# Performance work log

Measured on AMD Instinct MI355X. Metric: run time of the kernel, lower is better.

The kernel has to match this reference:

```python
import jax, jax.numpy as jnp
import numpy as np

# Whisper-small decoder, prefill path (text_offset == 0, no KV caches)
L, D, H, V, NCTX, S_AUDIO, B, T, MAXC = 12, 768, 12, 51865, 448, 1500, 2, 192, 256
DH = D // H
SCALE = DH ** -0.5
EPS = 1e-5

PNAMES = ['attn_ln_g', 'attn_ln_b', 'attn_q_w', 'attn_q_b', 'attn_k_w', 'attn_v_w', 'attn_v_b',
          'attn_o_w', 'attn_o_b', 'cross_ln_g', 'cross_ln_b', 'cross_q_w', 'cross_q_b',
          'cross_k_w', 'cross_v_w', 'cross_v_b', 'cross_o_w', 'cross_o_b',
          'mlp_ln_g', 'mlp_ln_b', 'mlp_w1', 'mlp_b1', 'mlp_w2', 'mlp_b2', 'ln_g', 'ln_b']


def _ln(x, g, b):
    m = jnp.mean(x, -1, keepdims=True)
    v = jnp.mean((x - m) ** 2, -1, keepdims=True)
    return (x - m) * jax.lax.rsqrt(v + EPS) * g + b


def _heads(t):
    b, t_, _ = t.shape
    return t.reshape(b, t_, H, DH).transpose(0, 2, 1, 3)  # (b,H,t,DH)


def _mha(q, k, v, mask):
    qh, kh, vh = _heads(q), _heads(k), _heads(v)
    qk = jnp.matmul(qh, kh.swapaxes(-1, -2)) * SCALE  # (B,H,Tq,Tk), broadcasts over kv batch 1
    if mask is not None:
        qk = qk + mask
    w = jax.nn.softmax(qk, axis=-1)
    o = jnp.matmul(w, vh)  # (B,H,Tq,DH)
    o = o.transpose(0, 2, 1, 3).reshape(q.shape[0], q.shape[1], D)
    return o, qk


def _lin(x, w, b=None):
    y = jnp.einsum('bti,oi->bto', x, w)
    return y if b is None else y + b


def _forward(x, xa, tok_emb, pos_emb, P):
    h = tok_emb[x] + pos_emb[:T]                        # (B,T,D)
    h = jnp.pad(h, ((0, 0), (0, MAXC - T), (0, 0)))     # pad to max_n_ctx_for_1st=256
    r = jnp.arange(MAXC)
    mask = jnp.where((r[None, :] > r[:, None]) | (r[None, :] >= T), -jnp.inf, 0.0)
    xa1 = xa[:1]                                        # xa.split(1)[0] in torch
    cross_qks, new_mkv, new_ckv = [], [], []
    for l in range(L):
        y = _ln(h, P['attn_ln_g'][l], P['attn_ln_b'][l])
        q = _lin(y, P['attn_q_w'][l], P['attn_q_b'][l])
        k = _lin(y, P['attn_k_w'][l])
        v = _lin(y, P['attn_v_w'][l], P['attn_v_b'][l])
        new_mkv += [k, v]
        o, _ = _mha(q, k, v, mask)
        h = h + _lin(o, P['attn_o_w'][l], P['attn_o_b'][l])
        y = _ln(h, P['cross_ln_g'][l], P['cross_ln_b'][l])
        q = _lin(y, P['cross_q_w'][l], P['cross_q_b'][l])
        ck = _lin(xa1, P['cross_k_w'][l])
        cv = _lin(xa1, P['cross_v_w'][l], P['cross_v_b'][l])
        new_ckv += [ck, cv]
        o, cqk = _mha(q, ck, cv, None)
        cross_qks.append(jax.lax.stop_gradient(cqk))    # qk.detach() in torch
        h = h + _lin(o, P['cross_o_w'][l], P['cross_o_b'][l])
        y = _ln(h, P['mlp_ln_g'][l], P['mlp_ln_b'][l])
        h = h + _lin(jax.nn.gelu(_lin(y, P['mlp_w1'][l], P['mlp_b1'][l]), approximate=False),
                     P['mlp_w2'][l], P['mlp_b2'][l])
    h = _ln(h, P['ln_g'], P['ln_b'])
    logits = jnp.matmul(h[:, :T], tok_emb.T).astype(jnp.float32)       # (B,T,V)
    cross_qks = jnp.concatenate(cross_qks, axis=0)[:, :, :T, :]        # (L*B,H,T,S_AUDIO)
    return logits, cross_qks, jnp.stack(new_mkv), jnp.stack(new_ckv)


def setup_inputs() -> dict:
    key = jax.random.key(0)
    ks = iter(jax.random.split(key, 48))
    def p(shape, s=0.02):
        return jax.random.normal(next(ks), shape, jnp.float32) * s
    inp = {
        'x': jax.random.randint(next(ks), (B, T), 0, V, dtype=jnp.int32),
        'xa': jax.random.normal(next(ks), (B, S_AUDIO, D), jnp.float32),
        'text_offset': 0,
        'isNewCKV': 1,
        'tok_emb': p((V, D)),
        'pos_emb': p((NCTX, D)),
        'attn_ln_g': 1.0 + p((L, D)), 'attn_ln_b': p((L, D)),
        'attn_q_w': p((L, D, D)), 'attn_q_b': p((L, D)),
        'attn_k_w': p((L, D, D)),
        'attn_v_w': p((L, D, D)), 'attn_v_b': p((L, D)),
        'attn_o_w': p((L, D, D)), 'attn_o_b': p((L, D)),
        'cross_ln_g': 1.0 + p((L, D)), 'cross_ln_b': p((L, D)),
        'cross_q_w': p((L, D, D)), 'cross_q_b': p((L, D)),
        'cross_k_w': p((L, D, D)),
        'cross_v_w': p((L, D, D)), 'cross_v_b': p((L, D)),
        'cross_o_w': p((L, D, D)), 'cross_o_b': p((L, D)),
        'mlp_ln_g': 1.0 + p((L, D)), 'mlp_ln_b': p((L, D)),
        'mlp_w1': p((L, 4 * D, D)), 'mlp_b1': p((L, 4 * D)),
        'mlp_w2': p((L, D, 4 * D)), 'mlp_b2': p((L, D)),
        'ln_g': 1.0 + p((D,)), 'ln_b': p((D,)),
    }
    return inp


def reference(x, xa, text_offset, isNewCKV, tok_emb, pos_emb,
              attn_ln_g, attn_ln_b, attn_q_w, attn_q_b, attn_k_w, attn_v_w, attn_v_b,
              attn_o_w, attn_o_b, cross_ln_g, cross_ln_b, cross_q_w, cross_q_b,
              cross_k_w, cross_v_w, cross_v_b, cross_o_w, cross_o_b,
              mlp_ln_g, mlp_ln_b, mlp_w1, mlp_b1, mlp_w2, mlp_b2, ln_g, ln_b):
    # text_offset == 0 prefill path; isNewCKV unused in the pure-python torch path
    P = dict(zip(PNAMES, (attn_ln_g, attn_ln_b, attn_q_w, attn_q_b, attn_k_w, attn_v_w, attn_v_b,
                          attn_o_w, attn_o_b, cross_ln_g, cross_ln_b, cross_q_w, cross_q_b,
                          cross_k_w, cross_v_w, cross_v_b, cross_o_w, cross_o_b,
                          mlp_ln_g, mlp_ln_b, mlp_w1, mlp_b1, mlp_w2, mlp_b2, ln_g, ln_b)))
    return _forward(x, xa, tok_emb, pos_emb, P)
```

## Files before the change

kernel.cpp:

```cpp
#include <hip/hip_runtime.h>
#include <math.h>

constexpr int kL = 12, kD = 768, kH = 12, kV = 51865, kSA = 1500;
constexpr int kB = 2, kT = 192, kMC = 256, kDH = 64;
constexpr float kScale = 0.125f;
constexpr float kEps = 1e-5f;
constexpr int kR = kB * kMC;
constexpr int kSLDc = 1504;

constexpr size_t SZ_LOGITS = (size_t)kB * kT * kV;
constexpr size_t SZ_CQK    = (size_t)kL * kB * kH * kT * kSA;
constexpr size_t SZ_MKV    = (size_t)2 * kL * kB * kMC * kD;
constexpr size_t OFF_CQK = SZ_LOGITS;
constexpr size_t OFF_MKV = OFF_CQK + SZ_CQK;
constexpr size_t OFF_CKV = OFF_MKV + SZ_MKV;

typedef float f32x4v __attribute__((ext_vector_type(4)));
typedef unsigned short us8v __attribute__((ext_vector_type(8)));
typedef unsigned short us4v __attribute__((ext_vector_type(4)));
typedef unsigned int   u32x4 __attribute__((ext_vector_type(4)));

static __device__ __forceinline__ unsigned short f2bf(float f) {
    unsigned int u = __float_as_uint(f);
    u += 0x7fffu + ((u >> 16) & 1u);
    return (unsigned short)(u >> 16);
}

static __device__ __forceinline__ unsigned int f2bf2(float lo, float hi) {
    unsigned int r;
    asm("v_cvt_pk_bf16_f32 %0, %1, %2" : "=v"(r) : "v"(lo), "v"(hi));
    return r;
}

static __device__ __forceinline__ float bf2f(unsigned short u) {
    return __uint_as_float((unsigned int)u << 16);
}

static __device__ __forceinline__ f32x4v mfma_bf16(us8v a, us8v b, f32x4v c) {
    asm("v_mfma_f32_16x16x32_bf16 %0, %1, %2, %0" : "+v"(c) : "v"(a), "v"(b));
    return c;
}

__global__ void k_embed(const int* __restrict__ x, const float* __restrict__ tok,
                        const float* __restrict__ pos, float* __restrict__ h)
{
    int idx = blockIdx.x * 256 + threadIdx.x;
    int d = idx % kD;
    int t = (idx / kD) % kMC;
    int b = idx / (kD * kMC);
    float v = 0.f;
    if (t < kT) {
        int tokid = x[b * kT + t];
        v = tok[(size_t)tokid * kD + d] + pos[(size_t)t * kD + d];
    }
    h[idx] = v;
}

__global__ void k_ln(const float* __restrict__ in, const float* __restrict__ g,
                     const float* __restrict__ bb, unsigned short* __restrict__ out)
{
    int r = blockIdx.x;
    const float* xr = in + (size_t)r * kD;
    int t = threadIdx.x;
    float x0 = xr[t], x1 = xr[t + 256], x2 = xr[t + 512];
    float s  = x0 + x1 + x2;
    float sq = x0 * x0 + x1 * x1 + x2 * x2;
    __shared__ float red[8];
    for (int o = 32; o > 0; o >>= 1) { s += __shfl_down(s, o); sq += __shfl_down(sq, o); }
    int w = t >> 6;
    if ((t & 63) == 0) { red[w] = s; red[4 + w] = sq; }
    __syncthreads();
    s  = red[0] + red[1] + red[2] + red[3];
    sq = red[4] + red[5] + red[6] + red[7];
    float m   = s * (1.f / kD);
    float var = sq * (1.f / kD) - m * m;
    float rs  = rsqrtf(var + kEps);
    unsigned short* orow = out + (size_t)r * kD;
    orow[t]       = f2bf((x0 - m) * rs * g[t]       + bb[t]);
    orow[t + 256] = f2bf((x1 - m) * rs * g[t + 256] + bb[t + 256]);
    orow[t + 512] = f2bf((x2 - m) * rs * g[t + 512] + bb[t + 512]);
}

__global__ void k_finalln(const float* __restrict__ h, const float* __restrict__ g,
                          const float* __restrict__ bb, unsigned short* __restrict__ out)
{
    int r = blockIdx.x;
    int b = r / kT, tt = r % kT;
    const float* xr = h + (size_t)(b * kMC + tt) * kD;
    int t = threadIdx.x;
    float x0 = xr[t], x1 = xr[t + 256], x2 = xr[t + 512];
    float s  = x0 + x1 + x2;
    float sq = x0 * x0 + x1 * x1 + x2 * x2;
    __shared__ float red[8];
    for (int o = 32; o > 0; o >>= 1) { s += __shfl_down(s, o); sq += __shfl_down(sq, o); }
    int w = t >> 6;
    if ((t & 63) == 0) { red[w] = s; red[4 + w] = sq; }
    __syncthreads();
    s  = red[0] + red[1] + red[2] + red[3];
    sq = red[4] + red[5] + red[6] + red[7];
    float m   = s * (1.f / kD);
    float var = sq * (1.f / kD) - m * m;
    float rs  = rsqrtf(var + kEps);
    unsigned short* orow = out + (size_t)r * kD;
    orow[t]       = f2bf((x0 - m) * rs * g[t]       + bb[t]);
    orow[t + 256] = f2bf((x1 - m) * rs * g[t + 256] + bb[t + 256]);
    orow[t + 512] = f2bf((x2 - m) * rs * g[t + 512] + bb[t + 512]);
}

struct GEntry { const float* W; const float* bias; const float* res; void* out; };
struct GBatch { GEntry e[24]; };

template <int ABF, int OBF>
__global__ __launch_bounds__(256)
void gemm_t(const void* __restrict__ Av, GBatch gb, int M, int N, int K,
            int dogelu)
{
    constexpr int LD = 72;
    __shared__ unsigned short As[3][64][LD];
    __shared__ unsigned short Ws[3][64][LD];
    const GEntry ge = gb.e[blockIdx.z];
    const float* __restrict__ W = ge.W;
    int bn = blockIdx.y * 64;
    int bm = blockIdx.x * 64;
    int tid = threadIdx.x;
    int wid = tid >> 6, lane = tid & 63;
    int wm = (wid >> 1) * 32, wn = (wid & 1) * 32;
    int l15 = lane & 15, lg = lane >> 4;
    int r = tid >> 2, cq = (tid & 3) * 16;
    int gr = bm + r, gc = bn + r;

    auto load_a = [&](int k0, u32x4& p0, u32x4& p1) {
        p0 = (u32x4){}; p1 = (u32x4){};
        if (ABF) {
            if (gr < M) {
                const unsigned short* ar =
                    (const unsigned short*)Av + (size_t)gr * K + k0 + cq;
                p0 = *(const u32x4*)ar;
                p1 = *(const u32x4*)(ar + 8);
            }
        } else {
            if (gr < M) {
                const float* ar = (const float*)Av + (size_t)gr * K + k0 + cq;
                float4 v0 = *(const float4*)(ar);
                float4 v1 = *(const float4*)(ar + 4);
                float4 v2 = *(const float4*)(ar + 8);
                float4 v3 = *(const float4*)(ar + 12);
                p0[0] = f2bf2(v0.x, v0.y); p0[1] = f2bf2(v0.z, v0.w);
                p0[2] = f2bf2(v1.x, v1.y); p0[3] = f2bf2(v1.z, v1.w);
                p1[0] = f2bf2(v2.x, v2.y); p1[1] = f2bf2(v2.z, v2.w);
                p1[2] = f2bf2(v3.x, v3.y); p1[3] = f2bf2(v3.z, v3.w);
            }
        }
    };
    auto load_w = [&](int k0, u32x4& p0, u32x4& p1) {
        p0 = (u32x4){}; p1 = (u32x4){};
        if (gc < N) {
            const float* wr = W + (size_t)gc * K + k0 + cq;
            float4 v0 = *(const float4*)(wr);
            float4 v1 = *(const float4*)(wr + 4);
            float4 v2 = *(const float4*)(wr + 8);
            float4 v3 = *(const float4*)(wr + 12);
            p0[0] = f2bf2(v0.x, v0.y); p0[1] = f2bf2(v0.z, v0.w);
            p0[2] = f2bf2(v1.x, v1.y); p0[3] = f2bf2(v1.z, v1.w);
            p1[0] = f2bf2(v2.x, v2.y); p1[1] = f2bf2(v2.z, v2.w);
            p1[2] = f2bf2(v3.x, v3.y); p1[3] = f2bf2(v3.z, v3.w);
        }
    };
    auto stage = [&](int buf, u32x4 a0, u32x4 a1, u32x4 w0, u32x4 w1) {
        *(u32x4*)&As[buf][r][cq]     = a0;
        *(u32x4*)&As[buf][r][cq + 8] = a1;
        *(u32x4*)&Ws[buf][r][cq]     = w0;
        *(u32x4*)&Ws[buf][r][cq + 8] = w1;
    };

    f32x4v acc00 = {}, acc01 = {}, acc10 = {}, acc11 = {};
    auto domfma = [&](int buf) {
        #pragma unroll
        for (int kc = 0; kc < 2; ++kc) {
            us8v af0 = *(const us8v*)&As[buf][wm + l15][kc * 32 + lg * 8];
            us8v af1 = *(const us8v*)&As[buf][wm + 16 + l15][kc * 32 + lg * 8];
            us8v wf0 = *(const us8v*)&Ws[buf][wn + l15][kc * 32 + lg * 8];
            us8v wf1 = *(const us8v*)&Ws[buf][wn + 16 + l15][kc * 32 + lg * 8];
            acc00 = mfma_bf16(af0, wf0, acc00);
            acc01 = mfma_bf16(af0, wf1, acc01);
            acc10 = mfma_bf16(af1, wf0, acc10);
            acc11 = mfma_bf16(af1, wf1, acc11);
        }
    };

    u32x4 a0A, a1A, w0A, w1A, a0B, a1B, w0B, w1B;
    load_a(0, a0A, a1A); load_w(0, w0A, w1A);
    stage(0, a0A, a1A, w0A, w1A);
    load_a(64, a0B, a1B); load_w(64, w0B, w1B);
    __syncthreads();

    int cur = 0;
    for (int k0 = 0; k0 < K; k0 += 128) {
        int n1 = cur + 1; if (n1 == 3) n1 = 0;
        int n2 = n1 + 1; if (n2 == 3) n2 = 0;
        if (k0 + 128 < K) { load_a(k0 + 128, a0A, a1A); load_w(k0 + 128, w0A, w1A); }
        domfma(cur);
        stage(n1, a0B, a1B, w0B, w1B);
        __syncthreads();
        if (k0 + 192 < K) { load_a(k0 + 192, a0B, a1B); load_w(k0 + 192, w0B, w1B); }
        domfma(n1);
        if (k0 + 128 < K) {
            stage(n2, a0A, a1A, w0A, w1A);
            __syncthreads();
        }
        cur = n2;
    }

    const float* bias = ge.bias;
    const float* res  = ge.res;
    f32x4v accs[2][2] = { { acc00, acc01 }, { acc10, acc11 } };
    #pragma unroll
    for (int fi = 0; fi < 2; ++fi) {
        #pragma unroll
        for (int fj = 0; fj < 2; ++fj) {
            int col = bn + wn + fj * 16 + l15;
            if (col >= N) continue;
            float bv = bias ? bias[col] : 0.f;
            #pragma unroll
            for (int rr = 0; rr < 4; ++rr) {
                int row = bm + wm + fi * 16 + lg * 4 + rr;
                if (row >= M) continue;
                float v = accs[fi][fj][rr] + bv;
                if (dogelu) v = 0.5f * v * (1.f + erff(v * 0.70710678118654752f));
                if (OBF) {
                    ((unsigned short*)ge.out)[(size_t)row * N + col] = f2bf(v);
                } else {
                    if (res) v += res[(size_t)row * N + col];
                    ((float*)ge.out)[(size_t)row * N + col] = v;
                }
            }
        }
    }
}

__global__ __launch_bounds__(256)
void k_logits(const unsigned short* __restrict__ A, const float* __restrict__ W,
              float* __restrict__ out)
{
    constexpr int LD = 72;
    __shared__ unsigned short As[64][LD];
    __shared__ unsigned short Ws[2][64][LD];
    int bn = blockIdx.x * 64;
    int tid = threadIdx.x;
    int wid = tid >> 6, lane = tid & 63;
    int wm = (wid >> 1) * 32, wn = (wid & 1) * 32;
    int l15 = lane & 15, lg = lane >> 4;
    int r = tid >> 2, cq = (tid & 3) * 16;
    int gc = bn + r;

    auto load_w = [&](int k0, u32x4& p0, u32x4& p1) {
        p0 = (u32x4){}; p1 = (u32x4){};
        if (gc < kV) {
            const float* wr = W + (size_t)gc * kD + k0 + cq;
            float4 v0 = *(const float4*)(wr);
            float4 v1 = *(const float4*)(wr + 4);
            float4 v2 = *(const float4*)(wr + 8);
            float4 v3 = *(const float4*)(wr + 12);
            p0[0] = f2bf2(v0.x, v0.y); p0[1] = f2bf2(v0.z, v0.w);
            p0[2] = f2bf2(v1.x, v1.y); p0[3] = f2bf2(v1.z, v1.w);
            p1[0] = f2bf2(v2.x, v2.y); p1[1] = f2bf2(v2.z, v2.w);
            p1[2] = f2bf2(v3.x, v3.y); p1[3] = f2bf2(v3.z, v3.w);
        }
    };

    f32x4v acc[6][4];
    #pragma unroll
    for (int i = 0; i < 6; ++i)
        #pragma unroll
        for (int j = 0; j < 4; ++j) acc[i][j] = (f32x4v){};

    u32x4 rw0, rw1;
    load_w(0, rw0, rw1);
    *(u32x4*)&Ws[0][r][cq]     = rw0;
    *(u32x4*)&Ws[0][r][cq + 8] = rw1;
    __syncthreads();

    int cur = 0;
    for (int k0 = 0; k0 < kD; k0 += 64) {
        bool more = (k0 + 64) < kD;
        if (more) load_w(k0 + 64, rw0, rw1);
        #pragma unroll
        for (int mt = 0; mt < 6; ++mt) {
            {
                const unsigned short* ar = A + (size_t)(mt * 64 + r) * kD + k0 + cq;
                us8v v0 = *(const us8v*)ar;
                us8v v1 = *(const us8v*)(ar + 8);
                *(us8v*)&As[r][cq]     = v0;
                *(us8v*)&As[r][cq + 8] = v1;
            }
            __syncthreads();
            #pragma unroll
            for (int kc = 0; kc < 2; ++kc) {
                us8v af0 = *(const us8v*)&As[wm + l15][kc * 32 + lg * 8];
                us8v af1 = *(const us8v*)&As[wm + 16 + l15][kc * 32 + lg * 8];
                us8v wf0 = *(const us8v*)&Ws[cur][wn + l15][kc * 32 + lg * 8];
                us8v wf1 = *(const us8v*)&Ws[cur][wn + 16 + l15][kc * 32 + lg * 8];
                acc[mt][0] = mfma_bf16(af0, wf0, acc[mt][0]);
                acc[mt][1] = mfma_bf16(af0, wf1, acc[mt][1]);
                acc[mt][2] = mfma_bf16(af1, wf0, acc[mt][2]);
                acc[mt][3] = mfma_bf16(af1, wf1, acc[mt][3]);
            }
            __syncthreads();
        }
        if (more) {
            int nxt = cur ^ 1;
            *(u32x4*)&Ws[nxt][r][cq]     = rw0;
            *(u32x4*)&Ws[nxt][r][cq + 8] = rw1;
            cur = nxt;
        }
    }
    #pragma unroll
    for (int mt = 0; mt < 6; ++mt) {
        #pragma unroll
        for (int fi = 0; fi < 2; ++fi) {
            #pragma unroll
            for (int fj = 0; fj < 2; ++fj) {
                int col = bn + wn + fj * 16 + l15;
                if (col >= kV) continue;
                #pragma unroll
                for (int rr = 0; rr < 4; ++rr) {
                    int row = mt * 64 + wm + fi * 16 + lg * 4 + rr;
                    out[(size_t)row * kV + col] = acc[mt][fi * 2 + fj][rr];
                }
            }
        }
    }
}

template <int QBF>
__global__ __launch_bounds__(256)
void k_scores(const void* __restrict__ qv, const float* __restrict__ kk,
              unsigned short* __restrict__ sws, float* __restrict__ cqk,
              int Nk, int sld, int selfmask, int kPerB)
{
    constexpr int LD = 72;
    __shared__ unsigned short As[64][LD];
    __shared__ unsigned short Ks[64][LD];
    int z = blockIdx.z, b = z / kH, h = z % kH;
    int bm = blockIdx.x * 64, bn = blockIdx.y * 64;
    const float* kbase = kk + (kPerB ? (size_t)b * kMC * kD : 0) + (size_t)h * kDH;

    int tid = threadIdx.x;
    int r = tid >> 2, c0 = (tid & 3) * 16;
    {
        if (QBF) {
            const unsigned short* q = (const unsigned short*)qv;
            const unsigned short* qr =
                q + (size_t)(b * kMC + bm + r) * kD + h * kDH + c0;
            *(us8v*)&As[r][c0]     = *(const us8v*)qr;
            *(us8v*)&As[r][c0 + 8] = *(const us8v*)(qr + 8);
        } else {
            const float* q = (const float*)qv;
            const float* qr = q + (size_t)(b * kMC + bm + r) * kD + h * kDH + c0;
            float4 v0 = *(const float4*)(qr);
            float4 v1 = *(const float4*)(qr + 4);
            float4 v2 = *(const float4*)(qr + 8);
            float4 v3 = *(const float4*)(qr + 12);
            u32x4 p0, p1;
            p0[0] = f2bf2(v0.x, v0.y); p0[1] = f2bf2(v0.z, v0.w);
            p0[2] = f2bf2(v1.x, v1.y); p0[3] = f2bf2(v1.z, v1.w);
            p1[0] = f2bf2(v2.x, v2.y); p1[1] = f2bf2(v2.z, v2.w);
            p1[2] = f2bf2(v3.x, v3.y); p1[3] = f2bf2(v3.z, v3.w);
            *(u32x4*)&As[r][c0]     = p0;
            *(u32x4*)&As[r][c0 + 8] = p1;
        }
        int gk = bn + r;
        if (gk < Nk) {
            const float* kr = kbase + (size_t)gk * kD + c0;
            float4 v0 = *(const float4*)(kr);
            float4 v1 = *(const float4*)(kr + 4);
            float4 v2 = *(const float4*)(kr + 8);
            float4 v3 = *(const float4*)(kr + 12);
            u32x4 p0, p1;
            p0[0] = f2bf2(v0.x, v0.y); p0[1] = f2bf2(v0.z, v0.w);
            p0[2] = f2bf2(v1.x, v1.y); p0[3] = f2bf2(v1.z, v1.w);
            p1[0] = f2bf2(v2.x, v2.y); p1[1] = f2bf2(v2.z, v2.w);
            p1[2] = f2bf2(v3.x, v3.y); p1[3] = f2bf2(v3.z, v3.w);
            *(u32x4*)&Ks[r][c0]     = p0;
            *(u32x4*)&Ks[r][c0 + 8] = p1;
        } else {
            u32x4 zz = {};
            *(u32x4*)&Ks[r][c0]     = zz;
            *(u32x4*)&Ks[r][c0 + 8] = zz;
        }
    }
    __syncthreads();

    int wid = tid >> 6, lane = tid & 63;
    int wm = (wid >> 1) * 32, wn = (wid & 1) * 32;
    int l15 = lane & 15, lg = lane >> 4;

    f32x4v acc[2][2] = {};
    #pragma unroll
    for (int kc = 0; kc < 2; ++kc) {
        us8v a0 = *(const us8v*)&As[wm + l15][kc * 32 + lg * 8];
        us8v a1 = *(const us8v*)&As[wm + 16 + l15][kc * 32 + lg * 8];
        us8v b0 = *(const us8v*)&Ks[wn + l15][kc * 32 + lg * 8];
        us8v b1 = *(const us8v*)&Ks[wn + 16 + l15][kc * 32 + lg * 8];
        acc[0][0] = mfma_bf16(a0, b0, acc[0][0]);
        acc[0][1] = mfma_bf16(a0, b1, acc[0][1]);
        acc[1][0] = mfma_bf16(a1, b0, acc[1][0]);
        acc[1][1] = mfma_bf16(a1, b1, acc[1][1]);
    }

    #pragma unroll
    for (int fm = 0; fm < 2; ++fm) {
        #pragma unroll
        for (int fn = 0; fn < 2; ++fn) {
            int gj = bn + wn + fn * 16 + l15;
            if (gj >= Nk) continue;
            #pragma unroll
            for (int rr = 0; rr < 4; ++rr) {
                int gi = bm + wm + fm * 16 + lg * 4 + rr;
                float val = acc[fm][fn][rr] * kScale;
                if (cqk && gi < kT)
                    cqk[(((size_t)(b * kH + h)) * kT + gi) * kSA + gj] = val;
                if (selfmask && (gj > gi || gj >= kT)) val = -1e30f;
                sws[((size_t)z * kMC + gi) * sld + gj] = f2bf(val);
            }
        }
    }
}

constexpr int kCH  = 128;
constexpr int kLDK = 136;
__global__ __launch_bounds__(256)
void k_pv(const unsigned short* __restrict__ sws, const float* __restrict__ vv,
          unsigned short* __restrict__ o, int Nk, int sld, int vPerB)
{
    __shared__ unsigned short Pb[16][kLDK];
    __shared__ unsigned short Vt[64][kLDK];
    __shared__ float smx[16], sinv[16];
    int z = blockIdx.y, b = z / kH, h = z % kH;
    int i0 = blockIdx.x * 16;
    int t = threadIdx.x, wid = t >> 6, lane = t & 63;
    int l15 = lane & 15, lg = lane >> 4;
    const float* vbase = vv + (vPerB ? (size_t)b * kMC * kD : 0) + (size_t)h * kDH;

    for (int r2 = wid; r2 < 16; r2 += 4) {
        const unsigned short* srow2 = sws + ((size_t)z * kMC + i0 + r2) * sld;
        float mx = -3e38f;
        for (int j0 = lane * 8; j0 < Nk; j0 += 512) {
            us8v v = *(const us8v*)&srow2[j0];
            #pragma unroll
            for (int e = 0; e < 8; ++e)
                if (j0 + e < Nk) mx = fmaxf(mx, bf2f(v[e]));
        }
        for (int off = 32; off > 0; off >>= 1) mx = fmaxf(mx, __shfl_xor(mx, off));
        float sum = 0.f;
        for (int j0 = lane * 8; j0 < Nk; j0 += 512) {
            us8v v = *(const us8v*)&srow2[j0];
            #pragma unroll
            for (int e = 0; e < 8; ++e)
                if (j0 + e < Nk) sum += expf(bf2f(v[e]) - mx);
        }
        for (int off = 32; off > 0; off >>= 1) sum += __shfl_xor(sum, off);
        if (lane == 0) { smx[r2] = mx; sinv[r2] = 1.f / sum; }
    }
    __syncthreads();

    int pr = t >> 4;
    int jb = (t & 15) * 8;
    const unsigned short* srow = sws + ((size_t)z * kMC + i0 + pr) * sld;
    float mxv = smx[pr];

    f32x4v acc = {};
    for (int k0 = 0; k0 < Nk; k0 += kCH) {
        #pragma unroll
        for (int u = 0; u < 4; ++u) {
            int flat = t + u * 256;
            int kr = (flat >> 4) * 2;
            int c4 = flat & 15;
            float4 va = {0,0,0,0}, vb2 = {0,0,0,0};
            if (k0 + kr < Nk)
                va = *(const float4*)(vbase + (size_t)(k0 + kr) * kD + c4 * 4);
            if (k0 + kr + 1 < Nk)
                vb2 = *(const float4*)(vbase + (size_t)(k0 + kr + 1) * kD + c4 * 4);
            *(unsigned int*)&Vt[c4 * 4 + 0][kr] = f2bf2(va.x, vb2.x);
            *(unsigned int*)&Vt[c4 * 4 + 1][kr] = f2bf2(va.y, vb2.y);
            *(unsigned int*)&Vt[c4 * 4 + 2][kr] = f2bf2(va.z, vb2.z);
            *(unsigned int*)&Vt[c4 * 4 + 3][kr] = f2bf2(va.w, vb2.w);
        }
        {
            us8v praw = *(const us8v*)&srow[k0 + jb];
            #pragma unroll
            for (int u = 0; u < 8; u += 2) {
                int gj0 = k0 + jb + u;
                float e0 = (gj0     < Nk) ? expf(bf2f(praw[u])     - mxv) : 0.f;
                float e1 = (gj0 + 1 < Nk) ? expf(bf2f(praw[u + 1]) - mxv) : 0.f;
                *(unsigned int*)&Pb[pr][jb + u] = f2bf2(e0, e1);
            }
        }
        __syncthreads();
        #pragma unroll
        for (int kc = 0; kc < 4; ++kc) {
            us8v a  = *(const us8v*)&Pb[l15][kc * 32 + lg * 8];
            us8v bf = *(const us8v*)&Vt[wid * 16 + l15][kc * 32 + lg * 8];
            acc = mfma_bf16(a, bf, acc);
        }
        __syncthreads();
    }

    #pragma unroll
    for (int rr = 0; rr < 4; ++rr) {
        int row = lg * 4 + rr;
        float v = acc[rr] * sinv[row];
        o[(size_t)(b * kMC + i0 + row) * kD + h * kDH + wid * 16 + l15] = f2bf(v);
    }
}

extern "C" void kernel_launch(void* const* d_in, const int* in_sizes, int n_in,
                              void* d_out, int out_size, void* d_ws, size_t ws_size,
                              hipStream_t stream)
{
    const int*   x   = (const int*)  d_in[0];
    const float* xa  = (const float*)d_in[1];
    const float* tok = (const float*)d_in[4];
    const float* pos = (const float*)d_in[5];
    const float* attn_ln_g  = (const float*)d_in[6];
    const float* attn_ln_b  = (const float*)d_in[7];
    const float* attn_q_w   = (const float*)d_in[8];
    const float* attn_q_b   = (const float*)d_in[9];
    const float* attn_k_w   = (const float*)d_in[10];
    const float* attn_v_w   = (const float*)d_in[11];
    const float* attn_v_b   = (const float*)d_in[12];
    const float* attn_o_w   = (const float*)d_in[13];
    const float* attn_o_b   = (const float*)d_in[14];
    const float* cross_ln_g = (const float*)d_in[15];
    const float* cross_ln_b = (const float*)d_in[16];
    const float* cross_q_w  = (const float*)d_in[17];
    const float* cross_q_b  = (const float*)d_in[18];
    const float* cross_k_w  = (const float*)d_in[19];
    const float* cross_v_w  = (const float*)d_in[20];
    const float* cross_v_b  = (const float*)d_in[21];
    const float* cross_o_w  = (const float*)d_in[22];
    const float* cross_o_b  = (const float*)d_in[23];
    const float* mlp_ln_g   = (const float*)d_in[24];
    const float* mlp_ln_b   = (const float*)d_in[25];
    const float* mlp_w1     = (const float*)d_in[26];
    const float* mlp_b1     = (const float*)d_in[27];
    const float* mlp_w2     = (const float*)d_in[28];
    const float* mlp_b2     = (const float*)d_in[29];
    const float* ln_g       = (const float*)d_in[30];
    const float* ln_b       = (const float*)d_in[31];

    float* out = (float*)d_out;
    float* h    = (float*)d_ws;
    float* qws  = h   + (size_t)kR * kD;
    unsigned short* sS    = (unsigned short*)(qws + (size_t)kR * kD);
    unsigned short* y16   = sS   + (size_t)kB * kH * kMC * kSLDc;
    unsigned short* qb16  = y16  + (size_t)kR * kD;
    unsigned short* o16   = qb16 + (size_t)kR * kD;
    unsigned short* hid16 = o16  + (size_t)kR * kD;
    unsigned short* yF16  = hid16 + (size_t)kR * 4 * kD;

    k_embed<<<kB * kMC * kD / 256, 256, 0, stream>>>(x, tok, pos, h);

    {
        GBatch gc{};
        for (int l = 0; l < kL; ++l) {
            gc.e[2 * l]     = { cross_k_w + (size_t)l * kD * kD, nullptr, nullptr,
                                out + OFF_CKV + (size_t)(2 * l) * kSA * kD };
            gc.e[2 * l + 1] = { cross_v_w + (size_t)l * kD * kD, cross_v_b + (size_t)l * kD,
                                nullptr,
                                out + OFF_CKV + (size_t)(2 * l + 1) * kSA * kD };
        }
        gemm_t<0, 0><<<dim3((kSA + 63) / 64, kD / 64, 2 * kL), 256, 0, stream>>>(
            xa, gc, kSA, kD, kD, 0);
    }

    for (int l = 0; l < kL; ++l) {
        size_t dd = (size_t)l * kD * kD;
        float* kbuf  = out + OFF_MKV + (size_t)(2 * l)     * kB * kMC * kD;
        float* vbuf  = out + OFF_MKV + (size_t)(2 * l + 1) * kB * kMC * kD;
        float* ckbuf = out + OFF_CKV + (size_t)(2 * l)     * kSA * kD;
        float* cvbuf = out + OFF_CKV + (size_t)(2 * l + 1) * kSA * kD;
        float* cqk   = out + OFF_CQK + (size_t)l * kB * kH * kT * kSA;

        k_ln<<<kR, 256, 0, stream>>>(h, attn_ln_g + l * kD, attn_ln_b + l * kD, y16);
        {
            GBatch g3{};
            g3.e[0] = { attn_q_w + dd, attn_q_b + (size_t)l * kD, nullptr, qws };
            g3.e[1] = { attn_k_w + dd, nullptr,                   nullptr, kbuf };
            g3.e[2] = { attn_v_w + dd, attn_v_b + (size_t)l * kD, nullptr, vbuf };
            gemm_t<1, 0><<<dim3(kR / 64, kD / 64, 3), 256, 0, stream>>>(
                y16, g3, kR, kD, kD, 0);
        }
        k_scores<0><<<dim3(kMC / 64, kMC / 64, kB * kH), 256, 0, stream>>>(
            qws, kbuf, sS, nullptr, kMC, kMC, 1, 1);
        k_pv<<<dim3(kMC / 16, kB * kH), 256, 0, stream>>>(sS, vbuf, o16, kMC, kMC, 1);
        {
            GBatch g1{};
            g1.e[0] = { attn_o_w + dd, attn_o_b + (size_t)l * kD, h, h };
            gemm_t<1, 0><<<dim3(kR / 64, kD / 64, 1), 256, 0, stream>>>(
                o16, g1, kR, kD, kD, 0);
        }

        k_ln<<<kR, 256, 0, stream>>>(h, cross_ln_g + l * kD, cross_ln_b + l * kD, y16);
        {
            GBatch g1{};
            g1.e[0] = { cross_q_w + dd, cross_q_b + (size_t)l * kD, nullptr, qb16 };
            gemm_t<1, 1><<<dim3(kR / 64, kD / 64, 1), 256, 0, stream>>>(
                y16, g1, kR, kD, kD, 0);
        }
        k_scores<1><<<dim3(kMC / 64, (kSA + 63) / 64, kB * kH), 256, 0, stream>>>(
            qb16, ckbuf, sS, cqk, kSA, kSLDc, 0, 0);
        k_pv<<<dim3(kMC / 16, kB * kH), 256, 0, stream>>>(sS, cvbuf, o16, kSA, kSLDc, 0);
        {
            GBatch g1{};
            g1.e[0] = { cross_o_w + dd, cross_o_b + (size_t)l * kD, h, h };
            gemm_t<1, 0><<<dim3(kR / 64, kD / 64, 1), 256, 0, stream>>>(
                o16, g1, kR, kD, kD, 0);
        }

        k_ln<<<kR, 256, 0, stream>>>(h, mlp_ln_g + l * kD, mlp_ln_b + l * kD, y16);
        {
            GBatch g1{};
            g1.e[0] = { mlp_w1 + (size_t)l * 4 * kD * kD, mlp_b1 + (size_t)l * 4 * kD,
                        nullptr, hid16 };
            gemm_t<1, 1><<<dim3(kR / 64, 4 * kD / 64, 1), 256, 0, stream>>>(
                y16, g1, kR, 4 * kD, kD, 1);
        }
        {
            GBatch g1{};
            g1.e[0] = { mlp_w2 + (size_t)l * 4 * kD * kD, mlp_b2 + (size_t)l * kD, h, h };
            gemm_t<1, 0><<<dim3(kR / 64, kD / 64, 1), 256, 0, stream>>>(
                hid16, g1, kR, kD, 4 * kD, 0);
        }
    }

    k_finalln<<<kB * kT, 256, 0, stream>>>(h, ln_g, ln_b, yF16);
    k_logits<<<dim3((kV + 63) / 64), 256, 0, stream>>>(yF16, tok, out);
}
```

Measured before the change: 3.325 ms.

## Split cross-attn scores kernel with K-tile reuse across query tiles; widen PV row blocks

Adds a dedicated cross-attention scores kernel where each block loads and converts one 64-row K tile once and loops over all four query tiles, instead of reloading and reconverting K per query tile. The self-attention scores kernel is specialised with the masking and strides fixed. The PV kernel now processes 32 query rows per block with two MFMA accumulators that share each V tile, halving the V reload and conversion work. The risks are lower parallelism (fewer blocks) and serialized query-tile loops with extra syncs.

```diff
diff --git a/kernel.cpp b/kernel.cpp
--- a/kernel.cpp
+++ b/kernel.cpp
@@ -332,62 +332,45 @@
     }
 }
 
-template <int QBF>
 __global__ __launch_bounds__(256)
-void k_scores(const void* __restrict__ qv, const float* __restrict__ kk,
-              unsigned short* __restrict__ sws, float* __restrict__ cqk,
-              int Nk, int sld, int selfmask, int kPerB)
+void k_scores(const float* __restrict__ q, const float* __restrict__ kk,
+              unsigned short* __restrict__ sws)
 {
     constexpr int LD = 72;
     __shared__ unsigned short As[64][LD];
     __shared__ unsigned short Ks[64][LD];
     int z = blockIdx.z, b = z / kH, h = z % kH;
     int bm = blockIdx.x * 64, bn = blockIdx.y * 64;
-    const float* kbase = kk + (kPerB ? (size_t)b * kMC * kD : 0) + (size_t)h * kDH;
+    const float* kbase = kk + (size_t)b * kMC * kD + (size_t)h * kDH;
 
     int tid = threadIdx.x;
     int r = tid >> 2, c0 = (tid & 3) * 16;
     {
-        if (QBF) {
-            const unsigned short* q = (const unsigned short*)qv;
-            const unsigned short* qr =
-                q + (size_t)(b * kMC + bm + r) * kD + h * kDH + c0;
-            *(us8v*)&As[r][c0]     = *(const us8v*)qr;
-            *(us8v*)&As[r][c0 + 8] = *(const us8v*)(qr + 8);
-        } else {
-            const float* q = (const float*)qv;
-            const float* qr = q + (size_t)(b * kMC + bm + r) * kD + h * kDH + c0;
-            float4 v0 = *(const float4*)(qr);
-            float4 v1 = *(const float4*)(qr + 4);
-            float4 v2 = *(const float4*)(qr + 8);
-            float4 v3 = *(const float4*)(qr + 12);
-            u32x4 p0, p1;
-            p0[0] = f2bf2(v0.x, v0.y); p0[1] = f2bf2(v0.z, v0.w);
-            p0[2] = f2bf2(v1.x, v1.y); p0[3] = f2bf2(v1.z, v1.w);
-            p1[0] = f2bf2(v2.x, v2.y); p1[1] = f2bf2(v2.z, v2.w);
-            p1[2] = f2bf2(v3.x, v3.y); p1[3] = f2bf2(v3.z, v3.w);
-            *(u32x4*)&As[r][c0]     = p0;
-            *(u32x4*)&As[r][c0 + 8] = p1;
-        }
-        int gk = bn + r;
-        if (gk < Nk) {
-            const float* kr = kbase + (size_t)gk * kD + c0;
-            float4 v0 = *(const float4*)(kr);
-            float4 v1 = *(const float4*)(kr + 4);
-            float4 v2 = *(const float4*)(kr + 8);
-            float4 v3 = *(const float4*)(kr + 12);
-            u32x4 p0, p1;
-            p0[0] = f2bf2(v0.x, v0.y); p0[1] = f2bf2(v0.z, v0.w);
-            p0[2] = f2bf2(v1.x, v1.y); p0[3] = f2bf2(v1.z, v1.w);
-            p1[0] = f2bf2(v2.x, v2.y); p1[1] = f2bf2(v2.z, v2.w);
-            p1[2] = f2bf2(v3.x, v3.y); p1[3] = f2bf2(v3.z, v3.w);
-            *(u32x4*)&Ks[r][c0]     = p0;
-            *(u32x4*)&Ks[r][c0 + 8] = p1;
-        } else {
-            u32x4 zz = {};
-            *(u32x4*)&Ks[r][c0]     = zz;
-            *(u32x4*)&Ks[r][c0 + 8] = zz;
-        }
+        const float* qr = q + (size_t)(b * kMC + bm + r) * kD + h * kDH + c0;
+        float4 v0 = *(const float4*)(qr);
+        float4 v1 = *(const float4*)(qr + 4);
+        float4 v2 = *(const float4*)(qr + 8);
+        float4 v3 = *(const float4*)(qr + 12);
+        u32x4 p0, p1;
+        p0[0] = f2bf2(v0.x, v0.y); p0[1] = f2bf2(v0.z, v0.w);
+        p0[2] = f2bf2(v1.x, v1.y); p0[3] = f2bf2(v1.z, v1.w);
+        p1[0] = f2bf2(v2.x, v2.y); p1[1] = f2bf2(v2.z, v2.w);
+        p1[2] = f2bf2(v3.x, v3.y); p1[3] = f2bf2(v3.z, v3.w);
+        *(u32x4*)&As[r][c0]     = p0;
+        *(u32x4*)&As[r][c0 + 8] = p1;
+
+        const float* kr = kbase + (size_t)(bn + r) * kD + c0;
+        float4 k0 = *(const float4*)(kr);
+        float4 k1 = *(const float4*)(kr + 4);
+        float4 k2 = *(const float4*)(kr + 8);
+        float4 k3 = *(const float4*)(kr + 12);
+        u32x4 q0, q1;
+        q0[0] = f2bf2(k0.x, k0.y); q0[1] = f2bf2(k0.z, k0.w);
+        q0[2] = f2bf2(k1.x, k1.y); q0[3] = f2bf2(k1.z, k1.w);
+        q1[0] = f2bf2(k2.x, k2.y); q1[1] = f2bf2(k2.z, k2.w);
+        q1[2] = f2bf2(k3.x, k3.y); q1[3] = f2bf2(k3.z, k3.w);
+        *(u32x4*)&Ks[r][c0]     = q0;
+        *(u32x4*)&Ks[r][c0 + 8] = q1;
     }
     __syncthreads();
 
@@ -413,17 +396,94 @@
         #pragma unroll
         for (int fn = 0; fn < 2; ++fn) {
             int gj = bn + wn + fn * 16 + l15;
-            if (gj >= Nk) continue;
             #pragma unroll
             for (int rr = 0; rr < 4; ++rr) {
                 int gi = bm + wm + fm * 16 + lg * 4 + rr;
                 float val = acc[fm][fn][rr] * kScale;
-                if (cqk && gi < kT)
-                    cqk[(((size_t)(b * kH + h)) * kT + gi) * kSA + gj] = val;
-                if (selfmask && (gj > gi || gj >= kT)) val = -1e30f;
-                sws[((size_t)z * kMC + gi) * sld + gj] = f2bf(val);
-            }
-        }
+                if (gj > gi || gj >= kT) val = -1e30f;
+                sws[((size_t)z * kMC + gi) * kMC + gj] = f2bf(val);
+            }
+        }
+    }
+}
+
+__global__ __launch_bounds__(256)
+void k_xscores(const unsigned short* __restrict__ q, const float* __restrict__ ck,
+               unsigned short* __restrict__ sws, float* __restrict__ cqk)
+{
+    constexpr int LD = 72;
+    __shared__ unsigned short As[64][LD];
+    __shared__ unsigned short Ks[64][LD];
+    int z = blockIdx.y, b = z / kH, h = z % kH;
+    int bn = blockIdx.x * 64;
+    int tid = threadIdx.x;
+    int wid = tid >> 6, lane = tid & 63;
+    int wm = (wid >> 1) * 32, wn = (wid & 1) * 32;
+    int l15 = lane & 15, lg = lane >> 4;
+    int r = tid >> 2, c0 = (tid & 3) * 16;
+
+    {
+        int gk = bn + r;
+        if (gk < kSA) {
+            const float* kr = ck + (size_t)gk * kD + h * kDH + c0;
+            float4 k0 = *(const float4*)(kr);
+            float4 k1 = *(const float4*)(kr + 4);
+            float4 k2 = *(const float4*)(kr + 8);
+            float4 k3 = *(const float4*)(kr + 12);
+            u32x4 q0, q1;
+            q0[0] = f2bf2(k0.x, k0.y); q0[1] = f2bf2(k0.z, k0.w);
+            q0[2] = f2bf2(k1.x, k1.y); q0[3] = f2bf2(k1.z, k1.w);
+            q1[0] = f2bf2(k2.x, k2.y); q1[1] = f2bf2(k2.z, k2.w);
+            q1[2] = f2bf2(k3.x, k3.y); q1[3] = f2bf2(k3.z, k3.w);
+            *(u32x4*)&Ks[r][c0]     = q0;
+            *(u32x4*)&Ks[r][c0 + 8] = q1;
+        } else {
+            u32x4 zz = {};
+            *(u32x4*)&Ks[r][c0]     = zz;
+            *(u32x4*)&Ks[r][c0 + 8] = zz;
+        }
+    }
+
+    for (int mt = 0; mt < 4; ++mt) {
+        int bm = mt * 64;
+        {
+            const unsigned short* qr =
+                q + (size_t)(b * kMC + bm + r) * kD + h * kDH + c0;
+            *(us8v*)&As[r][c0]     = *(const us8v*)qr;
+            *(us8v*)&As[r][c0 + 8] = *(const us8v*)(qr + 8);
+        }
+        __syncthreads();
+
+        f32x4v acc[2][2] = {};
+        #pragma unroll
+        for (int kc = 0; kc < 2; ++kc) {
+            us8v a0 = *(const us8v*)&As[wm + l15][kc * 32 + lg * 8];
+            us8v a1 = *(const us8v*)&As[wm + 16 + l15][kc * 32 + lg * 8];
+            us8v b0 = *(const us8v*)&Ks[wn + l15][kc * 32 + lg * 8];
+            us8v b1 = *(const us8v*)&Ks[wn + 16 + l15][kc * 32 + lg * 8];
+            acc[0][0] = mfma_bf16(a0, b0, acc[0][0]);
+            acc[0][1] = mfma_bf16(a0, b1, acc[0][1]);
+            acc[1][0] = mfma_bf16(a1, b0, acc[1][0]);
+            acc[1][1] = mfma_bf16(a1, b1, acc[1][1]);
+        }
+
+        #pragma unroll
+        for (int fm = 0; fm < 2; ++fm) {
+            #pragma unroll
+            for (int fn = 0; fn < 2; ++fn) {
+                int gj = bn + wn + fn * 16 + l15;
+                if (gj >= kSA) continue;
+                #pragma unroll
+                for (int rr = 0; rr < 4; ++rr) {
+                    int gi = bm + wm + fm * 16 + lg * 4 + rr;
+                    float val = acc[fm][fn][rr] * kScale;
+                    if (gi < kT)
+                        cqk[((size_t)z * kT + gi) * kSA + gj] = val;
+                    sws[((size_t)z * kMC + gi) * kSLDc + gj] = f2bf(val);
+                }
+            }
+        }
+        __syncthreads();
     }
 }
 
@@ -433,16 +493,16 @@
 void k_pv(const unsigned short* __restrict__ sws, const float* __restrict__ vv,
           unsigned short* __restrict__ o, int Nk, int sld, int vPerB)
 {
-    __shared__ unsigned short Pb[16][kLDK];
+    __shared__ unsigned short Pb[32][kLDK];
     __shared__ unsigned short Vt[64][kLDK];
-    __shared__ float smx[16], sinv[16];
+    __shared__ float smx[32], sinv[32];
     int z = blockIdx.y, b = z / kH, h = z % kH;
-    int i0 = blockIdx.x * 16;
+    int i0 = blockIdx.x * 32;
     int t = threadIdx.x, wid = t >> 6, lane = t & 63;
     int l15 = lane & 15, lg = lane >> 4;
     const float* vbase = vv + (vPerB ? (size_t)b * kMC * kD : 0) + (size_t)h * kDH;
 
-    for (int r2 = wid; r2 < 16; r2 += 4) {
+    for (int r2 = wid; r2 < 32; r2 += 4) {
         const unsigned short* srow2 = sws + ((size_t)z * kMC + i0 + r2) * sld;
         float mx = -3e38f;
         for (int j0 = lane * 8; j0 < Nk; j0 += 512) {
@@ -464,12 +524,12 @@
     }
     __syncthreads();
 
-    int pr = t >> 4;
-    int jb = (t & 15) * 8;
+    int pr = t >> 3;
+    int jb = (t & 7) * 16;
     const unsigned short* srow = sws + ((size_t)z * kMC + i0 + pr) * sld;
     float mxv = smx[pr];
 
-    f32x4v acc = {};
+    f32x4v acc0 = {}, acc1 = {};
     for (int k0 = 0; k0 < Nk; k0 += kCH) {
         #pragma unroll
         for (int u = 0; u < 4; ++u) {
@@ -487,30 +547,43 @@
             *(unsigned int*)&Vt[c4 * 4 + 3][kr] = f2bf2(va.w, vb2.w);
         }
         {
-            us8v praw = *(const us8v*)&srow[k0 + jb];
+            us8v praw0 = *(const us8v*)&srow[k0 + jb];
+            us8v praw1 = *(const us8v*)&srow[k0 + jb + 8];
             #pragma unroll
             for (int u = 0; u < 8; u += 2) {
                 int gj0 = k0 + jb + u;
-                float e0 = (gj0     < Nk) ? expf(bf2f(praw[u])     - mxv) : 0.f;
-                float e1 = (gj0 + 1 < Nk) ? expf(bf2f(praw[u + 1]) - mxv) : 0.f;
+                float e0 = (gj0     < Nk) ? expf(bf2f(praw0[u])     - mxv) : 0.f;
+                float e1 = (gj0 + 1 < Nk) ? expf(bf2f(praw0[u + 1]) - mxv) : 0.f;
                 *(unsigned int*)&Pb[pr][jb + u] = f2bf2(e0, e1);
             }
+            #pragma unroll
+            for (int u = 0; u < 8; u += 2) {
+                int gj0 = k0 + jb + 8 + u;
+                float e0 = (gj0     < Nk) ? expf(bf2f(praw1[u])     - mxv) : 0.f;
+                float e1 = (gj0 + 1 < Nk) ? expf(bf2f(praw1[u + 1]) - mxv) : 0.f;
+                *(unsigned int*)&Pb[pr][jb + 8 + u] = f2bf2(e0, e1);
+            }
         }
         __syncthreads();
         #pragma unroll
         for (int kc = 0; kc < 4; ++kc) {
-            us8v a  = *(const us8v*)&Pb[l15][kc * 32 + lg * 8];
             us8v bf = *(const us8v*)&Vt[wid * 16 + l15][kc * 32 + lg * 8];
-            acc = mfma_bf16(a, bf, acc);
+            us8v a0 = *(const us8v*)&Pb[l15][kc * 32 + lg * 8];
+            us8v a1 = *(const us8v*)&Pb[16 + l15][kc * 32 + lg * 8];
+            acc0 = mfma_bf16(a0, bf, acc0);
+            acc1 = mfma_bf16(a1, bf, acc1);
         }
         __syncthreads();
     }
 
     #pragma unroll
     for (int rr = 0; rr < 4; ++rr) {
-        int row = lg * 4 + rr;
-        float v = acc[rr] * sinv[row];
-        o[(size_t)(b * kMC + i0 + row) * kD + h * kDH + wid * 16 + l15] = f2bf(v);
+        int row0 = lg * 4 + rr;
+        int row1 = 16 + lg * 4 + rr;
+        o[(size_t)(b * kMC + i0 + row0) * kD + h * kDH + wid * 16 + l15] =
+            f2bf(acc0[rr] * sinv[row0]);
+        o[(size_t)(b * kMC + i0 + row1) * kD + h * kDH + wid * 16 + l15] =
+            f2bf(acc1[rr] * sinv[row1]);
     }
 }
 
@@ -591,9 +664,9 @@
             gemm_t<1, 0><<<dim3(kR / 64, kD / 64, 3), 256, 0, stream>>>(
                 y16, g3, kR, kD, kD, 0);
         }
-        k_scores<0><<<dim3(kMC / 64, kMC / 64, kB * kH), 256, 0, stream>>>(
-            qws, kbuf, sS, nullptr, kMC, kMC, 1, 1);
-        k_pv<<<dim3(kMC / 16, kB * kH), 256, 0, stream>>>(sS, vbuf, o16, kMC, kMC, 1);
+        k_scores<<<dim3(kMC / 64, kMC / 64, kB * kH), 256, 0, stream>>>(
+            qws, kbuf, sS);
+        k_pv<<<dim3(kMC / 32, kB * kH), 256, 0, stream>>>(sS, vbuf, o16, kMC, kMC, 1);
         {
             GBatch g1{};
             g1.e[0] = { attn_o_w + dd, attn_o_b + (size_t)l * kD, h, h };
@@ -608,9 +681,9 @@
             gemm_t<1, 1><<<dim3(kR / 64, kD / 64, 1), 256, 0, stream>>>(
                 y16, g1, kR, kD, kD, 0);
         }
-        k_scores<1><<<dim3(kMC / 64, (kSA + 63) / 64, kB * kH), 256, 0, stream>>>(
-            qb16, ckbuf, sS, cqk, kSA, kSLDc, 0, 0);
-        k_pv<<<dim3(kMC / 16, kB * kH), 256, 0, stream>>>(sS, cvbuf, o16, kSA, kSLDc, 0);
+        k_xscores<<<dim3((kSA + 63) / 64, kB * kH), 256, 0, stream>>>(
+            qb16, ckbuf, sS, cqk);
+        k_pv<<<dim3(kMC / 32, kB * kH), 256, 0, stream>>>(sS, cvbuf, o16, kSA, kSLDc, 0);
         {
             GBatch g1{};
             g1.e[0] = { cross_o_w + dd, cross_o_b + (size_t)l * kD, h, h };
```

Result: slower. 3.478 ms (+4.6%).

## Add 32-row triple-buffered bf16 GEMM for decoder layer projections

Applied to the files above, without the earlier changes.

Adds a new GEMM kernel with 32x64 output tiles and a three-stage shared-memory ring that prefetches two K-chunks ahead in registers. All per-layer projection and MLP GEMMs switch to it, doubling the block count on the 512-row problem so more CUs are busy, and overlapping global loads with MFMA work. The cost is that each weight tile is converted and loaded by twice as many blocks, which raises fp32 weight traffic and the amount of conversion work.

```diff
diff --git a/kernel.cpp b/kernel.cpp
--- a/kernel.cpp
+++ b/kernel.cpp
@@ -233,6 +233,110 @@
                     if (res) v += res[(size_t)row * N + col];
                     ((float*)ge.out)[(size_t)row * N + col] = v;
                 }
+            }
+        }
+    }
+}
+
+template <int OBF>
+__global__ __launch_bounds__(256)
+void gemm32(const unsigned short* __restrict__ A, GBatch gb, int M, int N, int K,
+            int dogelu)
+{
+    constexpr int LD = 72;
+    __shared__ unsigned short As[3][32][LD];
+    __shared__ unsigned short Ws[3][64][LD];
+    const GEntry ge = gb.e[blockIdx.z];
+    const float* __restrict__ W = ge.W;
+    int bn = blockIdx.y * 64;
+    int bm = blockIdx.x * 32;
+    int tid = threadIdx.x;
+    int wid = tid >> 6, lane = tid & 63;
+    int wr = (wid >> 1) * 16, wc = (wid & 1) * 32;
+    int l15 = lane & 15, lg = lane >> 4;
+    int ra = tid >> 3, ca = (tid & 7) * 8;
+    int rw = tid >> 2, cw = (tid & 3) * 16;
+    int gr = bm + ra, gc = bn + rw;
+
+    auto load_a = [&](int k0, us8v& p) {
+        p = (us8v){};
+        if (gr < M) p = *(const us8v*)(A + (size_t)gr * K + k0 + ca);
+    };
+    auto load_w = [&](int k0, u32x4& p0, u32x4& p1) {
+        p0 = (u32x4){}; p1 = (u32x4){};
+        if (gc < N) {
+            const float* wrp = W + (size_t)gc * K + k0 + cw;
+            float4 v0 = *(const float4*)(wrp);
+            float4 v1 = *(const float4*)(wrp + 4);
+            float4 v2 = *(const float4*)(wrp + 8);
+            float4 v3 = *(const float4*)(wrp + 12);
+            p0[0] = f2bf2(v0.x, v0.y); p0[1] = f2bf2(v0.z, v0.w);
+            p0[2] = f2bf2(v1.x, v1.y); p0[3] = f2bf2(v1.z, v1.w);
+            p1[0] = f2bf2(v2.x, v2.y); p1[1] = f2bf2(v2.z, v2.w);
+            p1[2] = f2bf2(v3.x, v3.y); p1[3] = f2bf2(v3.z, v3.w);
+        }
+    };
+    auto stage = [&](int buf, us8v a, u32x4 w0, u32x4 w1) {
+        *(us8v*)&As[buf][ra][ca]      = a;
+        *(u32x4*)&Ws[buf][rw][cw]     = w0;
+        *(u32x4*)&Ws[buf][rw][cw + 8] = w1;
+    };
+
+    f32x4v acc0 = {}, acc1 = {};
+    auto domfma = [&](int buf) {
+        #pragma unroll
+        for (int kc = 0; kc < 2; ++kc) {
+            us8v af  = *(const us8v*)&As[buf][wr + l15][kc * 32 + lg * 8];
+            us8v wf0 = *(const us8v*)&Ws[buf][wc + l15][kc * 32 + lg * 8];
+            us8v wf1 = *(const us8v*)&Ws[buf][wc + 16 + l15][kc * 32 + lg * 8];
+            acc0 = mfma_bf16(af, wf0, acc0);
+            acc1 = mfma_bf16(af, wf1, acc1);
+        }
+    };
+
+    us8v aA, aB;
+    u32x4 w0A, w1A, w0B, w1B;
+    load_a(0, aA); load_w(0, w0A, w1A);
+    stage(0, aA, w0A, w1A);
+    load_a(64, aB); load_w(64, w0B, w1B);
+    __syncthreads();
+
+    int cur = 0;
+    for (int k0 = 0; k0 < K; k0 += 128) {
+        int n1 = cur + 1; if (n1 == 3) n1 = 0;
+        int n2 = n1 + 1; if (n2 == 3) n2 = 0;
+        if (k0 + 128 < K) { load_a(k0 + 128, aA); load_w(k0 + 128, w0A, w1A); }
+        domfma(cur);
+        stage(n1, aB, w0B, w1B);
+        __syncthreads();
+        if (k0 + 192 < K) { load_a(k0 + 192, aB); load_w(k0 + 192, w0B, w1B); }
+        domfma(n1);
+        if (k0 + 128 < K) {
+            stage(n2, aA, w0A, w1A);
+            __syncthreads();
+        }
+        cur = n2;
+    }
+
+    const float* bias = ge.bias;
+    const float* res  = ge.res;
+    f32x4v accs[2] = { acc0, acc1 };
+    #pragma unroll
+    for (int fj = 0; fj < 2; ++fj) {
+        int col = bn + wc + fj * 16 + l15;
+        if (col >= N) continue;
+        float bv = bias ? bias[col] : 0.f;
+        #pragma unroll
+        for (int rr = 0; rr < 4; ++rr) {
+            int row = bm + wr + lg * 4 + rr;
+            if (row >= M) continue;
+            float v = accs[fj][rr] + bv;
+            if (dogelu) v = 0.5f * v * (1.f + erff(v * 0.70710678118654752f));
+            if (OBF) {
+                ((unsigned short*)ge.out)[(size_t)row * N + col] = f2bf(v);
+            } else {
+                if (res) v += res[(size_t)row * N + col];
+                ((float*)ge.out)[(size_t)row * N + col] = v;
             }
         }
     }
@@ -588,7 +692,7 @@
             g3.e[0] = { attn_q_w + dd, attn_q_b + (size_t)l * kD, nullptr, qws };
             g3.e[1] = { attn_k_w + dd, nullptr,                   nullptr, kbuf };
             g3.e[2] = { attn_v_w + dd, attn_v_b + (size_t)l * kD, nullptr, vbuf };
-            gemm_t<1, 0><<<dim3(kR / 64, kD / 64, 3), 256, 0, stream>>>(
+            gemm32<0><<<dim3(kR / 32, kD / 64, 3), 256, 0, stream>>>(
                 y16, g3, kR, kD, kD, 0);
         }
         k_scores<0><<<dim3(kMC / 64, kMC / 64, kB * kH), 256, 0, stream>>>(
@@ -597,7 +701,7 @@
         {
             GBatch g1{};
             g1.e[0] = { attn_o_w + dd, attn_o_b + (size_t)l * kD, h, h };
-            gemm_t<1, 0><<<dim3(kR / 64, kD / 64, 1), 256, 0, stream>>>(
+            gemm32<0><<<dim3(kR / 32, kD / 64, 1), 256, 0, stream>>>(
                 o16, g1, kR, kD, kD, 0);
         }
 
@@ -605,7 +709,7 @@
         {
             GBatch g1{};
             g1.e[0] = { cross_q_w + dd, cross_q_b + (size_t)l * kD, nullptr, qb16 };
-            gemm_t<1, 1><<<dim3(kR / 64, kD / 64, 1), 256, 0, stream>>>(
+            gemm32<1><<<dim3(kR / 32, kD / 64, 1), 256, 0, stream>>>(
                 y16, g1, kR, kD, kD, 0);
         }
         k_scores<1><<<dim3(kMC / 64, (kSA + 63) / 64, kB * kH), 256, 0, stream>>>(
@@ -614,7 +718,7 @@
         {
             GBatch g1{};
             g1.e[0] = { cross_o_w + dd, cross_o_b + (size_t)l * kD, h, h };
-            gemm_t<1, 0><<<dim3(kR / 64, kD / 64, 1), 256, 0, stream>>>(
+            gemm32<0><<<dim3(kR / 32, kD / 64, 1), 256, 0, stream>>>(
                 o16, g1, kR, kD, kD, 0);
         }
 
@@ -623,13 +727,13 @@
             GBatch g1{};
             g1.e[0] = { mlp_w1 + (size_t)l * 4 * kD * kD, mlp_b1 + (size_t)l * 4 * kD,
                         nullptr, hid16 };
-            gemm_t<1, 1><<<dim3(kR / 64, 4 * kD / 64, 1), 256, 0, stream>>>(
+            gemm32<1><<<dim3(kR / 32, 4 * kD / 64, 1), 256, 0, stream>>>(
                 y16, g1, kR, 4 * kD, kD, 1);
         }
         {
             GBatch g1{};
             g1.e[0] = { mlp_w2 + (size_t)l * 4 * kD * kD, mlp_b2 + (size_t)l * kD, h, h };
-            gemm_t<1, 0><<<dim3(kR / 64, kD / 64, 1), 256, 0, stream>>>(
+            gemm32<0><<<dim3(kR / 32, kD / 64, 1), 256, 0, stream>>>(
                 hid16, g1, kR, kD, 4 * kD, 0);
         }
     }
```

Measured after the change: 3.106 ms. 6.6% less time.
